# Performance work log

Measured on AMD Instinct MI355X. Metric: run time of the kernel, lower is better.

The kernel has to match this reference:

```python
import jax, jax.numpy as jnp
import numpy as np
from jax import lax

PAD = 40
MAX_DISP = 40
STRIDE2 = 1
CORR_MULT = 1.0


def _correlation1d(input1, input2):
    # input1, input2: [B, C, H, W]; kernel_size=1, stride1=1
    B, C, H, W = input1.shape
    D = 2 * MAX_DISP // STRIDE2 + 1  # 81 displacement channels
    # zero-pad input2 along the width dimension
    in2p = jnp.pad(input2, ((0, 0), (0, 0), (0, 0), (PAD, PAD)))
    offsets = jnp.arange(D, dtype=jnp.int32) * STRIDE2  # start col in padded map; disp = off - PAD

    def body(carry, off):
        shifted = lax.dynamic_slice(in2p, (0, 0, 0, off), (B, C, H, W))
        # mean over channels (sumelems = kernel_size^2 * C = C)
        c = jnp.sum(input1 * shifted, axis=1) / C  # [B, H, W]
        return carry, c

    _, corr = lax.scan(body, None, offsets)  # [D, B, H, W]
    out = jnp.transpose(corr, (1, 0, 2, 3)) * CORR_MULT  # [B, D, H, W]
    return out


def setup_inputs() -> dict:
    key = jax.random.key(0)
    k1, k2 = jax.random.split(key)
    input1 = jax.random.normal(k1, (8, 256, 96, 192), dtype=jnp.float32)
    input2 = jax.random.normal(k2, (8, 256, 96, 192), dtype=jnp.float32)
    return {"input1": input1, "input2": input2}


def reference(input1, input2):
    return _correlation1d(input1, input2)
```

## Files before the change

### kernel.cpp

```cpp
#include <hip/hip_runtime.h>


typedef __attribute__((ext_vector_type(8))) short short8;
typedef __attribute__((ext_vector_type(4))) float float4v;
typedef __attribute__((ext_vector_type(4))) int int4v;

__device__ __forceinline__ unsigned short f2bf(float f) {
  unsigned int u = __float_as_uint(f);
  return (unsigned short)((u + 0x7FFFu + ((u >> 16) & 1u)) >> 16);
}

__global__ __launch_bounds__(256, 3) void corr1d_kernel(
    const float* __restrict__ in1, const float* __restrict__ in2,
    float* __restrict__ out) {
  constexpr int W = 192, H = 96, C = 256, D = 81, PAD = 40;
  constexpr int HW = H * W;
  constexpr int KC = 32;
  constexpr int STR = 40;

  __shared__ __align__(16) unsigned short smem[18560];
  unsigned short* A_l = smem;
  unsigned short* B_l = smem + 192 * STR;
  float* E = (float*)smem;

  const int bh = blockIdx.x;
  const int b = bh / H;
  const int h = bh % H;
  const int tid = threadIdx.x;
  const int lane = tid & 63;
  const int wv = tid >> 6;
  const int l15 = lane & 15;
  const int lq = lane >> 4;

  for (int idx = tid; idx < 80 * 32; idx += 256) {
    int col = idx >> 5;
    int k = idx & 31;
    int j = (col < PAD) ? col : (W + col);
    B_l[j * STR + k] = 0;
  }

  float4v acc[3][6];
#pragma unroll
  for (int i = 0; i < 3; ++i)
#pragma unroll
    for (int jj = 0; jj < 6; ++jj)
      acc[i][jj] = (float4v){0.f, 0.f, 0.f, 0.f};

  const int base1 = (b * C * H + h) * W;

  for (int c0 = 0; c0 < C; c0 += KC) {
    __syncthreads();

    for (int t = tid; t < 384; t += 256) {
      const int isB = t >= 192;
      const int u = isB ? t - 192 : t;
      const float* src = isB ? in2 : in1;
      unsigned short* dst = isB ? (B_l + PAD * STR) : A_l;
      const int w0 = 4 * (u % 48);
      const int co = 8 * (u / 48);
      const int g = base1 + (c0 + co) * HW + w0;
      float4v v[8];
#pragma unroll
      for (int i = 0; i < 8; ++i)
        v[i] = *(const float4v*)(src + g + i * HW);
#pragma unroll
      for (int x = 0; x < 4; ++x) {
        unsigned short o[8];
#pragma unroll
        for (int i = 0; i < 8; ++i) o[i] = f2bf(v[i][x]);
        *(int4v*)(dst + (w0 + x) * STR + co) = *(const int4v*)o;
      }
    }
    __syncthreads();

    short8 af[3];
#pragma unroll
    for (int i = 0; i < 3; ++i) {
      const int wt = 3 * wv + i;
      af[i] = *(const short8*)(A_l + (16 * wt + l15) * STR + 8 * lq);
    }
#pragma unroll
    for (int jt = 0; jt < 8; ++jt) {
      const int ja = 3 * wv + jt;
      short8 bf = *(const short8*)(B_l + (16 * ja + l15) * STR + 8 * lq);
#pragma unroll
      for (int i = 0; i < 3; ++i) {
        const int jj = jt - i;
        if (jj >= 0 && jj < 6)
          acc[i][jj] = __builtin_amdgcn_mfma_f32_16x16x32_bf16(
              af[i], bf, acc[i][jj], 0, 0, 0);
      }
    }
  }

  const float scale = 1.0f / 256.0f;
#pragma unroll
  for (int p = 0; p < 2; ++p) {
    __syncthreads();
    if ((wv >> 1) == p) {
#pragma unroll
      for (int i = 0; i < 3; ++i) {
        const int wt = 3 * wv + i;
#pragma unroll
        for (int jj = 0; jj < 6; ++jj) {
          const int j = 16 * (wt + jj) + l15;
#pragma unroll
          for (int r = 0; r < 4; ++r) {
            const int w = 16 * wt + 4 * lq + r;
            const int d = j - w;
            if (d >= 0 && d < D)
              E[d * 97 + (w - 96 * p)] = acc[i][jj][r] * scale;
          }
        }
      }
    }
    __syncthreads();
    float* outp = out + (b * D * H + h) * W + 96 * p;
    for (int idx = tid; idx < D * 96; idx += 256) {
      const int d = idx / 96;
      const int w = idx - d * 96;
      outp[d * HW + w] = E[d * 97 + w];
    }
  }
}

extern "C" void kernel_launch(void* const* d_in, const int* in_sizes, int n_in,
                              void* d_out, int out_size, void* d_ws, size_t ws_size,
                              hipStream_t stream) {
  const float* in1 = (const float*)d_in[0];
  const float* in2 = (const float*)d_in[1];
  float* out = (float*)d_out;
  (void)in_sizes; (void)n_in; (void)out_size; (void)d_ws; (void)ws_size;
  corr1d_kernel<<<dim3(768), dim3(256), 0, stream>>>(in1, in2, out);
}
```

Before: 328.7 us.

## Split each row across four single-wave blocks to drop block-level syncs

Each (b,h) row is now handled by four 64-thread blocks, each owning a 48-column chunk. The in1 tile is loaded straight into registers and converted to bf16 there instead of being staged in LDS, and each block stages only its 128-column in2 window. With one wave per block, all __syncthreads are removed, and the output is written with vectorized float4 stores. In exchange, the overlapping in2 halo is loaded and converted redundantly across neighbouring blocks (128 columns per 48-column chunk), and the A loads are strided scalar global loads.

```diff
diff --git a/kernel.cpp b/kernel.cpp
--- a/kernel.cpp
+++ b/kernel.cpp
@@ -10,85 +10,99 @@
   return (unsigned short)((u + 0x7FFFu + ((u >> 16) & 1u)) >> 16);
 }
 
-__global__ __launch_bounds__(256, 3) void corr1d_kernel(
+__global__ __launch_bounds__(64, 3) void corr1d_kernel(
     const float* __restrict__ in1, const float* __restrict__ in2,
     float* __restrict__ out) {
-  constexpr int W = 192, H = 96, C = 256, D = 81, PAD = 40;
+  constexpr int W = 192, H = 96, C = 256, D = 81;
   constexpr int HW = H * W;
   constexpr int KC = 32;
-  constexpr int STR = 40;
+  constexpr int SB = 40;
+  constexpr int WCH = 48;
 
-  __shared__ __align__(16) unsigned short smem[18560];
-  unsigned short* A_l = smem;
-  unsigned short* B_l = smem + 192 * STR;
+  __shared__ __align__(16) unsigned short smem[128 * SB];
+  unsigned short* B_l = smem;
   float* E = (float*)smem;
 
-  const int bh = blockIdx.x;
+  const int bx = blockIdx.x;
+  const int q  = bx & 3;
+  const int bh = bx >> 2;
   const int b = bh / H;
   const int h = bh % H;
-  const int tid = threadIdx.x;
-  const int lane = tid & 63;
-  const int wv = tid >> 6;
+  const int lane = threadIdx.x;
   const int l15 = lane & 15;
-  const int lq = lane >> 4;
+  const int lq  = lane >> 4;
 
-  for (int idx = tid; idx < 80 * 32; idx += 256) {
-    int col = idx >> 5;
-    int k = idx & 31;
-    int j = (col < PAD) ? col : (W + col);
-    B_l[j * STR + k] = 0;
+  const int w0abs = WCH * q;
+  const int lo = (w0abs - 40 > 0) ? (w0abs - 40) : 0;
+  const int hi = (w0abs + 88 < W) ? (w0abs + 88) : W;
+  const int nbg = (hi - lo) >> 2;
+  const int jr0 = lo + 40 - w0abs;
+
+  if (q == 0) {
+    for (int t = lane; t < 160; t += 64) {
+      int j = t >> 2, kg = t & 3;
+      *(int4v*)(B_l + j * SB + kg * 8) = (int4v){0, 0, 0, 0};
+    }
+  } else if (q == 3) {
+    for (int t = lane; t < 160; t += 64) {
+      int j = 88 + (t >> 2), kg = t & 3;
+      *(int4v*)(B_l + j * SB + kg * 8) = (int4v){0, 0, 0, 0};
+    }
   }
 
   float4v acc[3][6];
 #pragma unroll
   for (int i = 0; i < 3; ++i)
 #pragma unroll
-    for (int jj = 0; jj < 6; ++jj)
-      acc[i][jj] = (float4v){0.f, 0.f, 0.f, 0.f};
+    for (int jj = 0; jj < 6; ++jj) acc[i][jj] = (float4v){0.f, 0.f, 0.f, 0.f};
 
-  const int base1 = (b * C * H + h) * W;
+  const int base = (b * C * H + h) * W;
+  const float* a_col = in1 + base + w0abs + l15;
+  const int ntasks = nbg * 4;
 
   for (int c0 = 0; c0 < C; c0 += KC) {
-    __syncthreads();
+    float a_raw[3][8];
+#pragma unroll
+    for (int i = 0; i < 3; ++i)
+#pragma unroll
+      for (int t = 0; t < 8; ++t)
+        a_raw[i][t] = a_col[(c0 + 8 * lq + t) * HW + 16 * i];
 
-    for (int t = tid; t < 384; t += 256) {
-      const int isB = t >= 192;
-      const int u = isB ? t - 192 : t;
-      const float* src = isB ? in2 : in1;
-      unsigned short* dst = isB ? (B_l + PAD * STR) : A_l;
-      const int w0 = 4 * (u % 48);
-      const int co = 8 * (u / 48);
-      const int g = base1 + (c0 + co) * HW + w0;
+    for (int t = lane; t < ntasks; t += 64) {
+      const int cg = t & 3;
+      const int wg = t >> 2;
+      const int gaddr = base + (c0 + cg * 8) * HW + lo + 4 * wg;
       float4v v[8];
 #pragma unroll
-      for (int i = 0; i < 8; ++i)
-        v[i] = *(const float4v*)(src + g + i * HW);
+      for (int i = 0; i < 8; ++i) v[i] = *(const float4v*)(in2 + gaddr + i * HW);
+      const int jr = jr0 + 4 * wg;
 #pragma unroll
       for (int x = 0; x < 4; ++x) {
         unsigned short o[8];
 #pragma unroll
         for (int i = 0; i < 8; ++i) o[i] = f2bf(v[i][x]);
-        *(int4v*)(dst + (w0 + x) * STR + co) = *(const int4v*)o;
+        *(int4v*)(B_l + (jr + x) * SB + cg * 8) = *(const int4v*)o;
       }
     }
-    __syncthreads();
 
     short8 af[3];
 #pragma unroll
     for (int i = 0; i < 3; ++i) {
-      const int wt = 3 * wv + i;
-      af[i] = *(const short8*)(A_l + (16 * wt + l15) * STR + 8 * lq);
+      unsigned short o[8];
+#pragma unroll
+      for (int t = 0; t < 8; ++t) o[t] = f2bf(a_raw[i][t]);
+      af[i] = *(const short8*)o;
     }
+
 #pragma unroll
     for (int jt = 0; jt < 8; ++jt) {
-      const int ja = 3 * wv + jt;
-      short8 bf = *(const short8*)(B_l + (16 * ja + l15) * STR + 8 * lq);
+      short8 bfr = *(const short8*)(B_l + (16 * jt + l15) * SB + 8 * lq);
 #pragma unroll
       for (int i = 0; i < 3; ++i) {
         const int jj = jt - i;
         if (jj >= 0 && jj < 6)
           acc[i][jj] = __builtin_amdgcn_mfma_f32_16x16x32_bf16(
-              af[i], bf, acc[i][jj], 0, 0, 0);
+              af[i], bfr, acc[i][jj], 0, 0, 0);
       }
     }
   }
@@ -96,30 +110,23 @@
   const float scale = 1.0f / 256.0f;
 #pragma unroll
   for (int p = 0; p < 2; ++p) {
-    __syncthreads();
-    if ((wv >> 1) == p) {
+    const int dlo = p ? 41 : 0;
+    const int nd  = p ? 40 : 41;
 #pragma unroll
-      for (int i = 0; i < 3; ++i) {
-        const int wt = 3 * wv + i;
+    for (int i = 0; i < 3; ++i)
 #pragma unroll
-        for (int jj = 0; jj < 6; ++jj) {
-          const int j = 16 * (wt + jj) + l15;
+      for (int jj = 0; jj < 6; ++jj)
 #pragma unroll
-          for (int r = 0; r < 4; ++r) {
-            const int w = 16 * wt + 4 * lq + r;
-            const int d = j - w;
-            if (d >= 0 && d < D)
-              E[d * 97 + (w - 96 * p)] = acc[i][jj][r] * scale;
-          }
+        for (int r = 0; r < 4; ++r) {
+          const int d  = 16 * jj + l15 - 4 * lq - r;
+          const int wr = 16 * i + 4 * lq + r;
+          if (d >= dlo && d < dlo + nd)
+            E[(d - dlo) * 48 + wr] = acc[i][jj][r] * scale;
         }
-      }
-    }
-    __syncthreads();
-    float* outp = out + (b * D * H + h) * W + 96 * p;
-    for (int idx = tid; idx < D * 96; idx += 256) {
-      const int d = idx / 96;
-      const int w = idx - d * 96;
-      outp[d * HW + w] = E[d * 97 + w];
+    for (int t = lane; t < nd * 12; t += 64) {
+      const int dr = t / 12, g = t % 12;
+      float4v val = *(const float4v*)(E + dr * 48 + 4 * g);
+      *(float4v*)(out + ((b * D + dlo + dr) * H + h) * W + w0abs + 4 * g) = val;
     }
   }
 }
@@ -131,5 +138,5 @@
   const float* in2 = (const float*)d_in[1];
   float* out = (float*)d_out;
   (void)in_sizes; (void)n_in; (void)out_size; (void)d_ws; (void)ws_size;
-  corr1d_kernel<<<dim3(768), dim3(256), 0, stream>>>(in1, in2, out);
+  corr1d_kernel<<<dim3(3072), dim3(64), 0, stream>>>(in1, in2, out);
 }
```

New measurement: 344.9 us. +5.0%, slower.

## Stage fp32 tiles via global_load_lds and convert to bf16 at fragment load

Applied to the files above, without the earlier changes.

Input tiles now go straight from global memory into LDS as fp32 using global_load_lds, which removes the register round-trip and the bf16 conversion during staging. The conversion to bf16 and the zero padding for out-of-range columns move into the MFMA fragment loads, which read LDS with a strided pattern. The epilogue writes the output by displacement halves using float4 stores over full rows. This doubles the LDS footprint, adds per-element conversion and strided LDS reads in the inner loop, and narrows the global loads from vector to 4-byte per lane.

```diff
diff --git a/kernel.cpp b/kernel.cpp
--- a/kernel.cpp
+++ b/kernel.cpp
@@ -3,72 +3,61 @@
 
 typedef __attribute__((ext_vector_type(8))) short short8;
 typedef __attribute__((ext_vector_type(4))) float float4v;
-typedef __attribute__((ext_vector_type(4))) int int4v;
 
 __device__ __forceinline__ unsigned short f2bf(float f) {
   unsigned int u = __float_as_uint(f);
   return (unsigned short)((u + 0x7FFFu + ((u >> 16) & 1u)) >> 16);
 }
 
+__device__ __forceinline__ void glds4(const float* g, float* l) {
+  __builtin_amdgcn_global_load_lds(
+      (const __attribute__((address_space(1))) void*)g,
+      (__attribute__((address_space(3))) void*)l, 4, 0, 0);
+}
+
 __global__ __launch_bounds__(256, 3) void corr1d_kernel(
     const float* __restrict__ in1, const float* __restrict__ in2,
     float* __restrict__ out) {
-  constexpr int W = 192, H = 96, C = 256, D = 81, PAD = 40;
+  constexpr int W = 192, H = 96, C = 256, D = 81;
   constexpr int HW = H * W;
   constexpr int KC = 32;
-  constexpr int STR = 40;
+  constexpr int SR = 194;
+  constexpr int ES = 196;
 
-  __shared__ __align__(16) unsigned short smem[18560];
-  unsigned short* A_l = smem;
-  unsigned short* B_l = smem + 192 * STR;
-  float* E = (float*)smem;
+  __shared__ __align__(16) float smem[2 * KC * SR];
+  float* As = smem;
+  float* Bs = smem + KC * SR;
+  float* E  = smem;
 
   const int bh = blockIdx.x;
-  const int b = bh / H;
-  const int h = bh % H;
+  const int b = bh / H, h = bh % H;
   const int tid = threadIdx.x;
   const int lane = tid & 63;
   const int wv = tid >> 6;
-  const int l15 = lane & 15;
-  const int lq = lane >> 4;
-
-  for (int idx = tid; idx < 80 * 32; idx += 256) {
-    int col = idx >> 5;
-    int k = idx & 31;
-    int j = (col < PAD) ? col : (W + col);
-    B_l[j * STR + k] = 0;
-  }
+  const int l15 = lane & 15, lq = lane >> 4;
+  const int base = (b * C * H + h) * W;
 
   float4v acc[3][6];
 #pragma unroll
   for (int i = 0; i < 3; ++i)
 #pragma unroll
-    for (int jj = 0; jj < 6; ++jj)
-      acc[i][jj] = (float4v){0.f, 0.f, 0.f, 0.f};
+    for (int jj = 0; jj < 6; ++jj) acc[i][jj] = (float4v){0.f, 0.f, 0.f, 0.f};
 
-  const int base1 = (b * C * H + h) * W;
-
-  for (int c0 = 0; c0 < C; c0 += KC) {
+  for (int m = 0; m < C / KC; ++m) {
+    const int c0 = KC * m;
     __syncthreads();
 
-    for (int t = tid; t < 384; t += 256) {
-      const int isB = t >= 192;
-      const int u = isB ? t - 192 : t;
-      const float* src = isB ? in2 : in1;
-      unsigned short* dst = isB ? (B_l + PAD * STR) : A_l;
-      const int w0 = 4 * (u % 48);
-      const int co = 8 * (u / 48);
-      const int g = base1 + (c0 + co) * HW + w0;
-      float4v v[8];
 #pragma unroll
-      for (int i = 0; i < 8; ++i)
-        v[i] = *(const float4v*)(src + g + i * HW);
+    for (int r = 0; r < 8; ++r) {
+      const int k = 8 * wv + r;
+      const float* g1 = in1 + base + (c0 + k) * HW + lane;
+      const float* g2 = in2 + base + (c0 + k) * HW + lane;
+      float* lA = As + k * SR;
+      float* lB = Bs + k * SR;
 #pragma unroll
-      for (int x = 0; x < 4; ++x) {
-        unsigned short o[8];
-#pragma unroll
-        for (int i = 0; i < 8; ++i) o[i] = f2bf(v[i][x]);
-        *(int4v*)(dst + (w0 + x) * STR + co) = *(const int4v*)o;
+      for (int g = 0; g < 3; ++g) {
+        glds4(g1 + 64 * g, lA + 64 * g);
+        glds4(g2 + 64 * g, lB + 64 * g);
       }
     }
     __syncthreads();
@@ -76,19 +65,30 @@
     short8 af[3];
 #pragma unroll
     for (int i = 0; i < 3; ++i) {
-      const int wt = 3 * wv + i;
-      af[i] = *(const short8*)(A_l + (16 * wt + l15) * STR + 8 * lq);
+      const float* ap = As + 48 * wv + 16 * i + l15;
+      unsigned short o[8];
+#pragma unroll
+      for (int t = 0; t < 8; ++t) o[t] = f2bf(ap[(8 * lq + t) * SR]);
+      af[i] = *(const short8*)o;
     }
 #pragma unroll
     for (int jt = 0; jt < 8; ++jt) {
-      const int ja = 3 * wv + jt;
-      short8 bf = *(const short8*)(B_l + (16 * ja + l15) * STR + 8 * lq);
+      const int j = 16 * (3 * wv + jt) + l15;
+      const bool ok = (j >= 40) && (j < 232);
+      const float* bp = Bs + (ok ? (j - 40) : 0);
+      unsigned short o[8];
+#pragma unroll
+      for (int t = 0; t < 8; ++t) {
+        float v = ok ? bp[(8 * lq + t) * SR] : 0.0f;
+        o[t] = f2bf(v);
+      }
+      short8 bfr = *(const short8*)o;
 #pragma unroll
       for (int i = 0; i < 3; ++i) {
         const int jj = jt - i;
         if (jj >= 0 && jj < 6)
           acc[i][jj] = __builtin_amdgcn_mfma_f32_16x16x32_bf16(
-              af[i], bf, acc[i][jj], 0, 0, 0);
+              af[i], bfr, acc[i][jj], 0, 0, 0);
       }
     }
   }
@@ -96,30 +96,25 @@
   const float scale = 1.0f / 256.0f;
 #pragma unroll
   for (int p = 0; p < 2; ++p) {
+    const int dlo = p ? 41 : 0;
+    const int nd  = p ? 40 : 41;
     __syncthreads();
-    if ((wv >> 1) == p) {
 #pragma unroll
-      for (int i = 0; i < 3; ++i) {
-        const int wt = 3 * wv + i;
+    for (int i = 0; i < 3; ++i)
 #pragma unroll
-        for (int jj = 0; jj < 6; ++jj) {
-          const int j = 16 * (wt + jj) + l15;
+      for (int jj = 0; jj < 6; ++jj)
 #pragma unroll
-          for (int r = 0; r < 4; ++r) {
-            const int w = 16 * wt + 4 * lq + r;
-            const int d = j - w;
-            if (d >= 0 && d < D)
-              E[d * 97 + (w - 96 * p)] = acc[i][jj][r] * scale;
-          }
+        for (int r = 0; r < 4; ++r) {
+          const int d = 16 * jj + l15 - 4 * lq - r;
+          const int w = 48 * wv + 16 * i + 4 * lq + r;
+          if (d >= dlo && d < dlo + nd)
+            E[(d - dlo) * ES + w] = acc[i][jj][r] * scale;
         }
-      }
-    }
     __syncthreads();
-    float* outp = out + (b * D * H + h) * W + 96 * p;
-    for (int idx = tid; idx < D * 96; idx += 256) {
-      const int d = idx / 96;
-      const int w = idx - d * 96;
-      outp[d * HW + w] = E[d * 97 + w];
+    for (int t = tid; t < nd * 48; t += 256) {
+      const int dr = t / 48, g = t % 48;
+      float4v val = *(const float4v*)(E + dr * ES + 4 * g);
+      *(float4v*)(out + ((b * D + dlo + dr) * H + h) * W + 4 * g) = val;
     }
   }
 }
```

New measurement: 325.5 us. No clear change (-1.0%).
